# Performance work log

Measured on AMD Instinct MI355X. Metric: run time of the kernel, lower is better.

Reference implementation:

```python
import jax, jax.numpy as jnp
import numpy as np

ALPHA = 1.5
A = 0.5
BANDWIDTH = 1.0
SPHERE_RADIUS = 1.0
HIDDEN = 1024
HEAD = 64
EPS_ACOS = 1e-07
EPS_NORM = 1e-12  # torch F.normalize clamp_min eps


def _l2norm(v):
    # F.normalize(v, p=2, dim=-1)
    n = jnp.sqrt(jnp.sum(v * v, axis=-1, keepdims=True))
    return v / jnp.maximum(n, EPS_NORM)


def setup_inputs() -> dict:
    key = jax.random.key(0)
    ks = jax.random.split(key, 7)
    B, S = 8, 2048
    s = 1.0 / np.sqrt(HIDDEN)
    return {
        "x": jax.random.normal(ks[0], (B, S, HIDDEN), dtype=jnp.float32),
        "Wq": jax.random.uniform(ks[1], (HIDDEN, HEAD), jnp.float32, -s, s),
        "bq": jax.random.uniform(ks[2], (HEAD,), jnp.float32, -s, s),
        "Wk": jax.random.uniform(ks[3], (HIDDEN, HEAD), jnp.float32, -s, s),
        "bk": jax.random.uniform(ks[4], (HEAD,), jnp.float32, -s, s),
        "Wv": jax.random.uniform(ks[5], (HIDDEN, HEAD), jnp.float32, -s, s),
        "bv": jax.random.uniform(ks[6], (HEAD,), jnp.float32, -s, s),
    }


def reference(x, Wq, bq, Wk, bk, Wv, bv):
    # q,k,v: [B,S,HEAD], L2-normalized along feature axis
    q = _l2norm(jnp.einsum("bsh,hd->bsd", x, Wq) + bq)
    k = _l2norm(jnp.einsum("bsh,hd->bsd", x, Wk) + bk)
    v = _l2norm(jnp.einsum("bsh,hd->bsd", x, Wv) + bv)

    # geodesic distance on sphere: [B,S,S]
    cos = jnp.einsum("bqd,bkd->bqk", q, k)
    g_dist = jnp.arccos(jnp.clip(cos, -1.0 + EPS_ACOS, 1.0 - EPS_ACOS)) * SPHERE_RADIUS

    # alpha < 2 -> power-law score
    score = (1.0 + g_dist / jnp.sqrt(BANDWIDTH)) ** (-HEAD - ALPHA)

    # dual degree normalization (a != 0): diag(row^-a) @ S @ diag(col^-a),
    # expressed as broadcast row/col scaling (same math, no diag_embed matmuls)
    r = jnp.sum(score, axis=-1) ** (-A)  # [B,Sq]
    c = jnp.sum(score, axis=-2) ** (-A)  # [B,Sk]
    k_tilde = r[..., :, None] * score * c[..., None, :]

    # L1 normalize over key axis (F.normalize p=1): entries are positive
    denom = jnp.maximum(jnp.sum(jnp.abs(k_tilde), axis=-1, keepdims=True), EPS_NORM)
    probs = k_tilde / denom

    out = jnp.einsum("bqk,bkd->bqd", probs, v)
    return (out, probs)
```

## Files before the change

kernel.cpp:

```cpp
#include <hip/hip_runtime.h>
#include <hip/hip_bf16.h>
#include <math.h>

#define BB 8
#define SS 2048
#define HH 1024
#define DD 64
#define NCV 65

typedef __attribute__((ext_vector_type(8))) short bf16x8;
typedef __attribute__((ext_vector_type(4))) float f32x4;
typedef __attribute__((ext_vector_type(16))) float f32x16;

#define MFMA16(a, b, c) __builtin_amdgcn_mfma_f32_16x16x32_bf16(a, b, c, 0, 0, 0)
#define MFMA32(a, b, c) __builtin_amdgcn_mfma_f32_32x32x16_bf16(a, b, c, 0, 0, 0)

__device__ __forceinline__ ushort bf16rne(float f) {
    uint u = __float_as_uint(f);
    uint r = (u + 0x7FFFu + ((u >> 16) & 1u)) >> 16;
    return (ushort)r;
}
__device__ __forceinline__ ushort bfc(float f) {
    __hip_bfloat16 h = __float2bfloat16(f);
    return *reinterpret_cast<ushort*>(&h);
}
__device__ __forceinline__ float bf2f(ushort h) {
    return __uint_as_float(((uint)h) << 16);
}

__device__ __forceinline__ float score_fn(float cosv) {
    float ax = fminf(fabsf(cosv), 1.0f - 1e-7f);
    float p = fmaf(ax, -0.0012624911f, 0.0066700901f);
    p = fmaf(ax, p, -0.0170881256f);
    p = fmaf(ax, p, 0.0308918810f);
    p = fmaf(ax, p, -0.0501743046f);
    p = fmaf(ax, p, 0.0889789874f);
    p = fmaf(ax, p, -0.2145988016f);
    p = fmaf(ax, p, 1.5707963050f);
    float r = sqrtf(1.0f - ax) * p;
    float g = (cosv >= 0.0f) ? r : (3.14159265358979f - r);
    return exp2f(-65.5f * log2f(1.0f + g));
}

__global__ __launch_bounds__(256) void k_prep(
    const float* __restrict__ Wq, const float* __restrict__ Wk, const float* __restrict__ Wv,
    const float* __restrict__ bq, const float* __restrict__ bk, const float* __restrict__ bv,
    ushort* __restrict__ Whi, ushort* __restrict__ Wlo, float* __restrict__ bcat)
{
    const int n = blockIdx.x;
    const int m = n >> 6, d = n & 63;
    const float* W = (m == 0) ? Wq : (m == 1 ? Wk : Wv);
    #pragma unroll
    for (int i = 0; i < 4; ++i) {
        int j = i * 256 + threadIdx.x;
        float f = W[(size_t)j * DD + d];
        ushort h = bf16rne(f);
        Whi[(size_t)n * HH + j] = h;
        Wlo[(size_t)n * HH + j] = bf16rne(f - bf2f(h));
    }
    if (n == 0 && threadIdx.x < 192) {
        int t = threadIdx.x, mm = t >> 6, dd = t & 63;
        const float* b = (mm == 0) ? bq : (mm == 1 ? bk : bv);
        bcat[t] = b[dd];
    }
}

__global__ __launch_bounds__(256) void k_projmm(
    const float* __restrict__ x, const ushort* __restrict__ Whi,
    const ushort* __restrict__ Wlo, const float* __restrict__ bcat,
    ushort* __restrict__ qh, ushort* __restrict__ ql,
    ushort* __restrict__ kh, ushort* __restrict__ kl,
    float* __restrict__ vw)
{
    __shared__ __align__(16) char smem[32 * 193 * 4];
    __shared__ float rns[96];
    __shared__ float bsh[192];
    ushort* xhi = (ushort*)smem;
    ushort* xlo = xhi + 32 * 128;
    float* ctile = (float*)smem;

    const int t = threadIdx.x;
    const int lane = t & 63;
    const int wid = t >> 6;
    const int row0 = blockIdx.x * 32;
    if (t < 192) bsh[t] = bcat[t];

    f32x4 acc[2][3];
    #pragma unroll
    for (int ar = 0; ar < 2; ++ar)
        #pragma unroll
        for (int bc = 0; bc < 3; ++bc)
            acc[ar][bc] = (f32x4){0.f, 0.f, 0.f, 0.f};

    for (int ch = 0; ch < 8; ++ch) {
        const int j0 = ch * 128;
        __syncthreads();
        #pragma unroll
        for (int i = 0; i < 2; ++i) {
            int u = i * 256 + t;
            int row = u >> 4, uc = u & 15;
            const float* xp = &x[(size_t)(row0 + row) * HH + j0 + uc * 8];
            float4 a = *(const float4*)xp;
            float4 b = *(const float4*)(xp + 4);
            float fs[8] = {a.x, a.y, a.z, a.w, b.x, b.y, b.z, b.w};
            bf16x8 hv, lv;
            #pragma unroll
            for (int e = 0; e < 8; ++e) {
                ushort h = bf16rne(fs[e]);
                hv[e] = (short)h;
                lv[e] = (short)bf16rne(fs[e] - bf2f(h));
            }
            int su = uc ^ (row & 7);
            *(bf16x8*)(xhi + row * 128 + su * 8) = hv;
            *(bf16x8*)(xlo + row * 128 + su * 8) = lv;
        }
        __syncthreads();
        #pragma unroll
        for (int ks = 0; ks < 4; ++ks) {
            bf16x8 ah[2], al[2], bh[3], bl[3];
            #pragma unroll
            for (int ar = 0; ar < 2; ++ar) {
                int row = ar * 16 + (lane & 15);
                int su = (ks * 4 + (lane >> 4)) ^ (row & 7);
                ah[ar] = *(const bf16x8*)(xhi + row * 128 + su * 8);
                al[ar] = *(const bf16x8*)(xlo + row * 128 + su * 8);
            }
            const int koff = j0 + ks * 32 + (lane >> 4) * 8;
            #pragma unroll
            for (int bc = 0; bc < 3; ++bc) {
                int n = wid * 48 + bc * 16 + (lane & 15);
                bh[bc] = *(const bf16x8*)(Whi + (size_t)n * HH + koff);
                bl[bc] = *(const bf16x8*)(Wlo + (size_t)n * HH + koff);
            }
            #pragma unroll
            for (int ar = 0; ar < 2; ++ar)
                #pragma unroll
                for (int bc = 0; bc < 3; ++bc) {
                    acc[ar][bc] = MFMA16(ah[ar], bh[bc], acc[ar][bc]);
                    acc[ar][bc] = MFMA16(ah[ar], bl[bc], acc[ar][bc]);
                    acc[ar][bc] = MFMA16(al[ar], bh[bc], acc[ar][bc]);
                }
        }
    }
    __syncthreads();
    #pragma unroll
    for (int ar = 0; ar < 2; ++ar)
        #pragma unroll
        for (int bc = 0; bc < 3; ++bc) {
            int n = wid * 48 + bc * 16 + (lane & 15);
            #pragma unroll
            for (int r = 0; r < 4; ++r) {
                int row = ar * 16 + (lane >> 4) * 4 + r;
                ctile[row * 193 + n] = acc[ar][bc][r];
            }
        }
    __syncthreads();
    if (t < 96) {
        int mat = t >> 5, row = t & 31;
        float ss = 0.f;
        #pragma unroll 8
        for (int d = 0; d < 64; ++d) {
            float v = ctile[row * 193 + mat * 64 + d] + bsh[mat * 64 + d];
            ss = fmaf(v, v, ss);
        }
        rns[t] = 1.0f / fmaxf(sqrtf(ss), 1e-12f);
    }
    __syncthreads();
    #pragma unroll
    for (int i = 0; i < 24; ++i) {
        int idx = i * 256 + t;
        int row = idx / 192;
        int n = idx - row * 192;
        float v = (ctile[row * 193 + n] + bsh[n]) * rns[(n >> 6) * 32 + row];
        size_t off = (size_t)(row0 + row) * DD + (n & 63);
        if (n < 64) {
            ushort h = bf16rne(v);
            qh[off] = h; ql[off] = bf16rne(v - bf2f(h));
        } else if (n < 128) {
            ushort h = bf16rne(v);
            kh[off] = h; kl[off] = bf16rne(v - bf2f(h));
        } else {
            vw[off] = v;
        }
    }
}

#define K_LOAD(H0,H1,H2,H3,L0,L1,L2,L3, KT) { \
    const ushort* kp = kh + (size_t)(b * SS + kbase + (KT) * 32 + qrow) * DD + kg; \
    const ushort* lp = kl + (size_t)(b * SS + kbase + (KT) * 32 + qrow) * DD + kg; \
    H0 = *(const bf16x8*)(kp);      L0 = *(const bf16x8*)(lp); \
    H1 = *(const bf16x8*)(kp + 16); L1 = *(const bf16x8*)(lp + 16); \
    H2 = *(const bf16x8*)(kp + 32); L2 = *(const bf16x8*)(lp + 32); \
    H3 = *(const bf16x8*)(kp + 48); L3 = *(const bf16x8*)(lp + 48); }

#define K_COMPUTE(H0,H1,H2,H3,L0,L1,L2,L3, KT) { \
    f32x16 acc = Z16; \
    acc = MFMA32(H0, qbh0, acc); acc = MFMA32(H0, qbl0, acc); acc = MFMA32(L0, qbh0, acc); \
    acc = MFMA32(H1, qbh1, acc); acc = MFMA32(H1, qbl1, acc); acc = MFMA32(L1, qbh1, acc); \
    acc = MFMA32(H2, qbh2, acc); acc = MFMA32(H2, qbl2, acc); acc = MFMA32(L2, qbh2, acc); \
    acc = MFMA32(H3, qbh3, acc); acc = MFMA32(H3, qbl3, acc); acc = MFMA32(L3, qbh3, acc); \
    const int kloc = kbase + (KT) * 32 + hi4; \
    uint2 wv; \
    wv.x = (uint)bfc(score_fn(acc[0]))  | ((uint)bfc(score_fn(acc[1]))  << 16); \
    wv.y = (uint)bfc(score_fn(acc[2]))  | ((uint)bfc(score_fn(acc[3]))  << 16); \
    *(uint2*)(srow + kloc) = wv; \
    wv.x = (uint)bfc(score_fn(acc[4]))  | ((uint)bfc(score_fn(acc[5]))  << 16); \
    wv.y = (uint)bfc(score_fn(acc[6]))  | ((uint)bfc(score_fn(acc[7]))  << 16); \
    *(uint2*)(srow + kloc + 8) = wv; \
    wv.x = (uint)bfc(score_fn(acc[8]))  | ((uint)bfc(score_fn(acc[9]))  << 16); \
    wv.y = (uint)bfc(score_fn(acc[10])) | ((uint)bfc(score_fn(acc[11])) << 16); \
    *(uint2*)(srow + kloc + 16) = wv; \
    wv.x = (uint)bfc(score_fn(acc[12])) | ((uint)bfc(score_fn(acc[13])) << 16); \
    wv.y = (uint)bfc(score_fn(acc[14])) | ((uint)bfc(score_fn(acc[15])) << 16); \
    *(uint2*)(srow + kloc + 24) = wv; }

__global__ __launch_bounds__(256, 4) void k_score(
    const ushort* __restrict__ qh, const ushort* __restrict__ ql,
    const ushort* __restrict__ kh, const ushort* __restrict__ kl,
    ushort* __restrict__ scrS)
{
    const int t = threadIdx.x;
    const int lane = t & 63;
    const int w = t >> 6;
    const int bid = blockIdx.x;
    const int b  = bid >> 8;
    const int q0 = ((bid >> 2) & 63) * 32;
    const int kbase = (bid & 3) * 512 + w * 128;
    const int qrow = lane & 31;
    const int kg = (lane >> 5) * 8;
    const int hi4 = (lane >> 5) * 4;
    const f32x16 Z16 = {0.f,0.f,0.f,0.f,0.f,0.f,0.f,0.f,0.f,0.f,0.f,0.f,0.f,0.f,0.f,0.f};

    const size_t qoff = (size_t)(b * SS + q0 + qrow) * DD + kg;
    bf16x8 qbh0 = *(const bf16x8*)(qh + qoff);
    bf16x8 qbh1 = *(const bf16x8*)(qh + qoff + 16);
    bf16x8 qbh2 = *(const bf16x8*)(qh + qoff + 32);
    bf16x8 qbh3 = *(const bf16x8*)(qh + qoff + 48);
    bf16x8 qbl0 = *(const bf16x8*)(ql + qoff);
    bf16x8 qbl1 = *(const bf16x8*)(ql + qoff + 16);
    bf16x8 qbl2 = *(const bf16x8*)(ql + qoff + 32);
    bf16x8 qbl3 = *(const bf16x8*)(ql + qoff + 48);
    ushort* srow = scrS + (size_t)(b * SS + q0 + qrow) * 4096 + 2048;

    bf16x8 xh0, xh1, xh2, xh3, xl0, xl1, xl2, xl3;
    bf16x8 yh0, yh1, yh2, yh3, yl0, yl1, yl2, yl3;
    K_LOAD(xh0,xh1,xh2,xh3,xl0,xl1,xl2,xl3, 0)
    K_LOAD(yh0,yh1,yh2,yh3,yl0,yl1,yl2,yl3, 1)
    K_COMPUTE(xh0,xh1,xh2,xh3,xl0,xl1,xl2,xl3, 0)
    K_LOAD(xh0,xh1,xh2,xh3,xl0,xl1,xl2,xl3, 2)
    K_COMPUTE(yh0,yh1,yh2,yh3,yl0,yl1,yl2,yl3, 1)
    K_LOAD(yh0,yh1,yh2,yh3,yl0,yl1,yl2,yl3, 3)
    K_COMPUTE(xh0,xh1,xh2,xh3,xl0,xl1,xl2,xl3, 2)
    K_COMPUTE(yh0,yh1,yh2,yh3,yl0,yl1,yl2,yl3, 3)
}

__global__ __launch_bounds__(256) void k_csum(
    const ushort* __restrict__ scrS, float* __restrict__ colsum)
{
    __shared__ float cls[32][64];
    const int t = threadIdx.x;
    const int bid = blockIdx.x;
    const int b  = bid >> 8;
    const int k0 = ((bid >> 3) & 31) * 64;
    const int qs = (bid & 7) * 256;
    const int tq = t >> 3, tk = t & 7;
    float colacc[8];
    #pragma unroll
    for (int e = 0; e < 8; ++e) colacc[e] = 0.f;
    #pragma unroll 2
    for (int it = 0; it < 8; ++it) {
        int q = qs + it * 32 + tq;
        bf16x8 s8 = *(const bf16x8*)(scrS + (size_t)(b * SS + q) * 4096 + 2048 + k0 + tk * 8);
        #pragma unroll
        for (int e = 0; e < 8; ++e) colacc[e] += bf2f((ushort)s8[e]);
    }
    #pragma unroll
    for (int e = 0; e < 8; ++e) cls[tq][tk * 8 + e] = colacc[e];
    __syncthreads();
    if (t < 64) {
        float s = 0.f;
        #pragma unroll
        for (int i = 0; i < 32; ++i) s += cls[i][t];
        atomicAdd(&colsum[b * SS + k0 + t], s);
    }
}

__global__ __launch_bounds__(256) void k_cvc(
    const float* __restrict__ vw, const float* __restrict__ colsum,
    ushort* __restrict__ cvT)
{
    __shared__ float vs[64][65];
    __shared__ float csh[64];
    const int t = threadIdx.x;
    const int b = blockIdx.x >> 5;
    const int k0 = (blockIdx.x & 31) * 64;
    #pragma unroll
    for (int i = 0; i < 4; ++i) {
        int idx = i * 256 + t;
        int r = idx >> 4, c4 = idx & 15;
        float4 v4 = *(const float4*)&vw[(size_t)(b * SS + k0 + r) * DD + c4 * 4];
        *(float4*)&vs[r][c4 * 4] = v4;
    }
    if (t < 64) csh[t] = 1.0f / sqrtf(colsum[b * SS + k0 + t]);
    __syncthreads();
    const int kk4 = (t & 15) * 4;
    #pragma unroll
    for (int jt = 0; jt < 4; ++jt) {
        int j = jt * 16 + (t >> 4);
        uint2 wv;
        wv.x = (uint)bfc(csh[kk4 + 0] * vs[kk4 + 0][j])
             | ((uint)bfc(csh[kk4 + 1] * vs[kk4 + 1][j]) << 16);
        wv.y = (uint)bfc(csh[kk4 + 2] * vs[kk4 + 2][j])
             | ((uint)bfc(csh[kk4 + 3] * vs[kk4 + 3][j]) << 16);
        *(uint2*)(cvT + ((size_t)b * NCV + j) * SS + k0 + kk4) = wv;
    }
    if (t < 16) {
        uint2 wv;
        wv.x = (uint)bfc(csh[t * 4 + 0]) | ((uint)bfc(csh[t * 4 + 1]) << 16);
        wv.y = (uint)bfc(csh[t * 4 + 2]) | ((uint)bfc(csh[t * 4 + 3]) << 16);
        *(uint2*)(cvT + ((size_t)b * NCV + 64) * SS + k0 + t * 4) = wv;
    }
}

__global__ __launch_bounds__(256, 4) void k_ndp(
    const ushort* __restrict__ scrS, const ushort* __restrict__ cvT,
    float* __restrict__ probs, float* __restrict__ out)
{
    __shared__ float nred[16][64];
    __shared__ float dPart[4][16];
    __shared__ float dInv[16];
    const int t = threadIdx.x;
    const int lane = t & 63;
    const int w = t >> 6;
    const int b = blockIdx.x >> 7;
    const int q0 = (blockIdx.x & 127) * 16;
    const int kbase = w * 512;
    const int qn = lane & 15;
    const int g = lane >> 4;

    ((float*)nred)[t] = 0.f; ((float*)nred)[t + 256] = 0.f;
    ((float*)nred)[t + 512] = 0.f; ((float*)nred)[t + 768] = 0.f;
    __syncthreads();

    const ushort* cslice = cvT + (size_t)b * NCV * SS;
    const ushort* cbrow = cslice + (size_t)64 * SS;

    float dacc = 0.f;
    f32x4 nacc[4];
    #pragma unroll
    for (int ct = 0; ct < 4; ++ct) nacc[ct] = (f32x4){0.f, 0.f, 0.f, 0.f};

    const ushort* sp = scrS + (size_t)(b * SS + q0 + qn) * 4096 + 2048 + kbase + g * 8;
    const ushort* cp = cbrow + kbase + g * 8;
    const ushort* p0 = cslice + (size_t)(0 * 16 + qn) * SS + kbase + g * 8;
    const ushort* p1 = cslice + (size_t)(1 * 16 + qn) * SS + kbase + g * 8;
    const ushort* p2 = cslice + (size_t)(2 * 16 + qn) * SS + kbase + g * 8;
    const ushort* p3 = cslice + (size_t)(3 * 16 + qn) * SS + kbase + g * 8;

    #pragma unroll 4
    for (int ch = 0; ch < 16; ++ch) {
        bf16x8 s8 = *(const bf16x8*)sp;
        bf16x8 c8 = *(const bf16x8*)cp;
        bf16x8 b0 = *(const bf16x8*)p0;
        bf16x8 b1 = *(const bf16x8*)p1;
        bf16x8 b2 = *(const bf16x8*)p2;
        bf16x8 b3 = *(const bf16x8*)p3;
        #pragma unroll
        for (int e = 0; e < 8; ++e)
            dacc = fmaf(bf2f((ushort)s8[e]), bf2f((ushort)c8[e]), dacc);
        nacc[0] = MFMA16(s8, b0, nacc[0]);
        nacc[1] = MFMA16(s8, b1, nacc[1]);
        nacc[2] = MFMA16(s8, b2, nacc[2]);
        nacc[3] = MFMA16(s8, b3, nacc[3]);
        sp += 32; cp += 32; p0 += 32; p1 += 32; p2 += 32; p3 += 32;
    }
    {
        float d = dacc;
        d += __shfl_xor(d, 16, 64);
        d += __shfl_xor(d, 32, 64);
        if (lane < 16) dPart[w][lane] = d;
    }
    __syncthreads();
    if (t < 16) dInv[t] = 1.0f / (dPart[0][t] + dPart[1][t] + dPart[2][t] + dPart[3][t]);
    #pragma unroll
    for (int ct = 0; ct < 4; ++ct)
        #pragma unroll
        for (int r = 0; r < 4; ++r)
            atomicAdd(&nred[g * 4 + r][ct * 16 + qn], nacc[ct][r]);
    __syncthreads();
    {
        int q = t >> 4, c4 = (t & 15) * 4;
        float di = dInv[q];
        float4 o;
        o.x = nred[q][c4] * di;     o.y = nred[q][c4 + 1] * di;
        o.z = nred[q][c4 + 2] * di; o.w = nred[q][c4 + 3] * di;
        *(float4*)&out[(size_t)(b * SS + q0 + q) * DD + c4] = o;
    }
    float cf[8];
    {
        bf16x8 c8 = *(const bf16x8*)(cbrow + t * 8);
        #pragma unroll
        for (int e = 0; e < 8; ++e) cf[e] = bf2f((ushort)c8[e]);
    }
    #pragma unroll
    for (int rb = 0; rb < 4; ++rb) {
        bf16x8 s[4];
        float dl[4];
        #pragma unroll
        for (int j = 0; j < 4; ++j) {
            int row = rb * 4 + j;
            s[j] = *(const bf16x8*)(scrS + (size_t)(b * SS + q0 + row) * 4096 + 2048 + t * 8);
            dl[j] = dInv[row];
        }
        __syncthreads();
        #pragma unroll
        for (int j = 0; j < 4; ++j) {
            f32x4 o0, o1;
            o0[0] = bf2f((ushort)s[j][0]) * cf[0] * dl[j];
            o0[1] = bf2f((ushort)s[j][1]) * cf[1] * dl[j];
            o0[2] = bf2f((ushort)s[j][2]) * cf[2] * dl[j];
            o0[3] = bf2f((ushort)s[j][3]) * cf[3] * dl[j];
            o1[0] = bf2f((ushort)s[j][4]) * cf[4] * dl[j];
            o1[1] = bf2f((ushort)s[j][5]) * cf[5] * dl[j];
            o1[2] = bf2f((ushort)s[j][6]) * cf[6] * dl[j];
            o1[3] = bf2f((ushort)s[j][7]) * cf[7] * dl[j];
            float* prow = probs + (size_t)(b * SS + q0 + rb * 4 + j) * SS + t * 8;
            __builtin_nontemporal_store(o0, (f32x4*)prow);
            __builtin_nontemporal_store(o1, (f32x4*)(prow + 4));
        }
    }
}

extern "C" void kernel_launch(void* const* d_in, const int* in_sizes, int n_in,
                              void* d_out, int out_size, void* d_ws, size_t ws_size,
                              hipStream_t stream)
{
    const float* x  = (const float*)d_in[0];
    const float* Wq = (const float*)d_in[1];
    const float* bq = (const float*)d_in[2];
    const float* Wk = (const float*)d_in[3];
    const float* bk = (const float*)d_in[4];
    const float* Wv = (const float*)d_in[5];
    const float* bv = (const float*)d_in[6];

    float* out   = (float*)d_out;
    float* probs = out + (size_t)BB * SS * DD;
    ushort* scrS = (ushort*)probs;

    const size_t NQ = (size_t)BB * SS * DD;
    ushort* qh    = (ushort*)d_ws;
    ushort* ql    = qh + NQ;
    ushort* kh    = ql + NQ;
    ushort* kl    = kh + NQ;
    float*  vw    = (float*)(kl + NQ);
    float*  colsum = vw + NQ;
    ushort* cvT   = (ushort*)(colsum + BB * SS);
    ushort* Whi   = cvT + (size_t)BB * NCV * SS;
    ushort* Wlo   = Whi + (size_t)192 * HH;
    float*  bcat  = (float*)(Wlo + (size_t)192 * HH);

    hipMemsetAsync(colsum, 0, BB * SS * sizeof(float), stream);
    k_prep  <<<192, 256, 0, stream>>>(Wq, Wk, Wv, bq, bk, bv, Whi, Wlo, bcat);
    k_projmm<<<512, 256, 0, stream>>>(x, Whi, Wlo, bcat, qh, ql, kh, kl, vw);
    k_score <<<2048, 256, 0, stream>>>(qh, ql, kh, kl, scrS);
    k_csum  <<<2048, 256, 0, stream>>>(scrS, colsum);
    k_cvc   <<<256, 256, 0, stream>>>(vw, colsum, cvT);
    k_ndp   <<<1024, 256, 0, stream>>>(scrS, cvT, probs, out);
}
```

Baseline: 224.6 us.

## Fuse column-sum into score kernel via swizzled LDS staging

The score kernel now writes its bf16 score tile into a swizzled 32KB shared-memory buffer and no longer stores straight to global. From there it computes per-column partial sums with atomics and writes the tile to global with coalesced 16-byte stores. This removes the separate k_csum kernel, which re-read the whole score matrix from global memory, and it also turns the scattered 8-byte global stores into wider coalesced ones. In exchange it adds 32KB of LDS per block, which may limit occupancy under the launch bound of 4, plus a block barrier.

```diff
diff --git a/kernel.cpp b/kernel.cpp
--- a/kernel.cpp
+++ b/kernel.cpp
@@ -199,36 +199,40 @@
     acc = MFMA32(H1, qbh1, acc); acc = MFMA32(H1, qbl1, acc); acc = MFMA32(L1, qbh1, acc); \
     acc = MFMA32(H2, qbh2, acc); acc = MFMA32(H2, qbl2, acc); acc = MFMA32(L2, qbh2, acc); \
     acc = MFMA32(H3, qbh3, acc); acc = MFMA32(H3, qbl3, acc); acc = MFMA32(L3, qbh3, acc); \
-    const int kloc = kbase + (KT) * 32 + hi4; \
+    const int kb = (w * 128 + (KT) * 32) * 2 + hi8; \
     uint2 wv; \
     wv.x = (uint)bfc(score_fn(acc[0]))  | ((uint)bfc(score_fn(acc[1]))  << 16); \
     wv.y = (uint)bfc(score_fn(acc[2]))  | ((uint)bfc(score_fn(acc[3]))  << 16); \
-    *(uint2*)(srow + kloc) = wv; \
+    *(uint2*)(ldsrow + ((kb +  0) ^ swq)) = wv; \
     wv.x = (uint)bfc(score_fn(acc[4]))  | ((uint)bfc(score_fn(acc[5]))  << 16); \
     wv.y = (uint)bfc(score_fn(acc[6]))  | ((uint)bfc(score_fn(acc[7]))  << 16); \
-    *(uint2*)(srow + kloc + 8) = wv; \
+    *(uint2*)(ldsrow + ((kb + 16) ^ swq)) = wv; \
     wv.x = (uint)bfc(score_fn(acc[8]))  | ((uint)bfc(score_fn(acc[9]))  << 16); \
     wv.y = (uint)bfc(score_fn(acc[10])) | ((uint)bfc(score_fn(acc[11])) << 16); \
-    *(uint2*)(srow + kloc + 16) = wv; \
+    *(uint2*)(ldsrow + ((kb + 32) ^ swq)) = wv; \
     wv.x = (uint)bfc(score_fn(acc[12])) | ((uint)bfc(score_fn(acc[13])) << 16); \
     wv.y = (uint)bfc(score_fn(acc[14])) | ((uint)bfc(score_fn(acc[15])) << 16); \
-    *(uint2*)(srow + kloc + 24) = wv; }
+    *(uint2*)(ldsrow + ((kb + 48) ^ swq)) = wv; }
 
 __global__ __launch_bounds__(256, 4) void k_score(
     const ushort* __restrict__ qh, const ushort* __restrict__ ql,
     const ushort* __restrict__ kh, const ushort* __restrict__ kl,
-    ushort* __restrict__ scrS)
-{
+    ushort* __restrict__ scrS, float* __restrict__ colsum)
+{
+    __shared__ __align__(16) char slds[32 * 1024];
     const int t = threadIdx.x;
     const int lane = t & 63;
     const int w = t >> 6;
     const int bid = blockIdx.x;
     const int b  = bid >> 8;
     const int q0 = ((bid >> 2) & 63) * 32;
-    const int kbase = (bid & 3) * 512 + w * 128;
+    const int kgB = (bid & 3) * 512;
+    const int kbase = kgB + w * 128;
     const int qrow = lane & 31;
     const int kg = (lane >> 5) * 8;
-    const int hi4 = (lane >> 5) * 4;
+    const int hi8 = (lane >> 5) * 8;
+    const int swq = (qrow & 15) << 3;
+    char* ldsrow = slds + qrow * 1024;
     const f32x16 Z16 = {0.f,0.f,0.f,0.f,0.f,0.f,0.f,0.f,0.f,0.f,0.f,0.f,0.f,0.f,0.f,0.f};
 
     const size_t qoff = (size_t)(b * SS + q0 + qrow) * DD + kg;
@@ -240,7 +244,6 @@
     bf16x8 qbl1 = *(const bf16x8*)(ql + qoff + 16);
     bf16x8 qbl2 = *(const bf16x8*)(ql + qoff + 32);
     bf16x8 qbl3 = *(const bf16x8*)(ql + qoff + 48);
-    ushort* srow = scrS + (size_t)(b * SS + q0 + qrow) * 4096 + 2048;
 
     bf16x8 xh0, xh1, xh2, xh3, xl0, xl1, xl2, xl3;
     bf16x8 yh0, yh1, yh2, yh3, yl0, yl1, yl2, yl3;
@@ -252,36 +255,34 @@
     K_LOAD(yh0,yh1,yh2,yh3,yl0,yl1,yl2,yl3, 3)
     K_COMPUTE(xh0,xh1,xh2,xh3,xl0,xl1,xl2,xl3, 2)
     K_COMPUTE(yh0,yh1,yh2,yh3,yl0,yl1,yl2,yl3, 3)
-}
-
-__global__ __launch_bounds__(256) void k_csum(
-    const ushort* __restrict__ scrS, float* __restrict__ colsum)
-{
-    __shared__ float cls[32][64];
-    const int t = threadIdx.x;
-    const int bid = blockIdx.x;
-    const int b  = bid >> 8;
-    const int k0 = ((bid >> 3) & 31) * 64;
-    const int qs = (bid & 7) * 256;
-    const int tq = t >> 3, tk = t & 7;
-    float colacc[8];
-    #pragma unroll
-    for (int e = 0; e < 8; ++e) colacc[e] = 0.f;
-    #pragma unroll 2
-    for (int it = 0; it < 8; ++it) {
-        int q = qs + it * 32 + tq;
-        bf16x8 s8 = *(const bf16x8*)(scrS + (size_t)(b * SS + q) * 4096 + 2048 + k0 + tk * 8);
-        #pragma unroll
-        for (int e = 0; e < 8; ++e) colacc[e] += bf2f((ushort)s8[e]);
-    }
-    #pragma unroll
-    for (int e = 0; e < 8; ++e) cls[tq][tk * 8 + e] = colacc[e];
-    __syncthreads();
-    if (t < 64) {
-        float s = 0.f;
-        #pragma unroll
-        for (int i = 0; i < 32; ++i) s += cls[i][t];
-        atomicAdd(&colsum[b * SS + k0 + t], s);
+
+    __syncthreads();
+    {
+        float s0 = 0.f, s1 = 0.f;
+        #pragma unroll 8
+        for (int r = 0; r < 32; ++r) {
+            uint d = *(const uint*)(slds + r * 1024 + ((t * 4) ^ ((r & 15) << 3)));
+            s0 += bf2f((ushort)(d & 0xFFFFu));
+            s1 += bf2f((ushort)(d >> 16));
+        }
+        atomicAdd(&colsum[b * SS + kgB + t * 2 + 0], s0);
+        atomicAdd(&colsum[b * SS + kgB + t * 2 + 1], s1);
+    }
+    {
+        const int r = t >> 3;
+        const int swr = (r & 15) << 3;
+        const char* lrow = slds + r * 1024;
+        ushort* srowg = scrS + (size_t)(b * SS + q0 + r) * 4096 + 2048 + kgB;
+        #pragma unroll
+        for (int i = 0; i < 8; ++i) {
+            int c = (t & 7) + i * 8;
+            int lc = c * 16;
+            uint2 a = *(const uint2*)(lrow + (lc ^ swr));
+            uint2 bb = *(const uint2*)(lrow + ((lc + 8) ^ swr));
+            uint4 v;
+            v.x = a.x; v.y = a.y; v.z = bb.x; v.w = bb.y;
+            *(uint4*)(srowg + c * 8) = v;
+        }
     }
 }
 
@@ -462,8 +463,7 @@
     hipMemsetAsync(colsum, 0, BB * SS * sizeof(float), stream);
     k_prep  <<<192, 256, 0, stream>>>(Wq, Wk, Wv, bq, bk, bv, Whi, Wlo, bcat);
     k_projmm<<<512, 256, 0, stream>>>(x, Whi, Wlo, bcat, qh, ql, kh, kl, vw);
-    k_score <<<2048, 256, 0, stream>>>(qh, ql, kh, kl, scrS);
-    k_csum  <<<2048, 256, 0, stream>>>(scrS, colsum);
+    k_score <<<2048, 256, 0, stream>>>(qh, ql, kh, kl, scrS, colsum);
     k_cvc   <<<256, 256, 0, stream>>>(vw, colsum, cvT);
     k_ndp   <<<1024, 256, 0, stream>>>(scrS, cvT, probs, out);
 }
```

Measured after the change: 191.1 us. 1.17x faster.
